# Kernel tuning notes

Measured on AMD Instinct MI355X. Metric: run time of the kernel, lower is better.

Reference implementation:

```python
import jax, jax.numpy as jnp
import numpy as np
import math

DIM = 1536
NH = 12
HD = 128          # head_dim
C = HD // 2       # 64 complex rope dims
MAX_ATTN = 15 * 880
EPS = 1e-6


def _rope_tables(max_len=1024, d=HD, theta=10000.0):
    # Wan rope_params: freqs = cat([rope(1024, d-4*(d//6)), rope(1024, 2*(d//6)), rope(1024, 2*(d//6))], dim=1)
    d0 = d - 4 * (d // 6)   # 44 -> 22 complex dims (F axis)
    d1 = 2 * (d // 6)       # 42 -> 21 complex dims (H and W axes)
    parts = []
    for dd in (d0, d1, d1):
        inv = 1.0 / theta ** (np.arange(0, dd, 2, dtype=np.float32) / dd)
        parts.append(np.outer(np.arange(max_len, dtype=np.float32), inv))
    ang = np.concatenate(parts, axis=1)                 # [1024, C]
    return np.stack([np.cos(ang), np.sin(ang)], -1)     # [1024, C, 2]


def rmsnorm(x, g, eps=EPS):
    return x * jax.lax.rsqrt(jnp.mean(x * x, axis=-1, keepdims=True) + eps) * g


def rope_apply(xq, f, h, w, freqs, start_frame):
    # xq: [B, S, N, D]; freqs: [1024, C, 2] cos/sin tables; S = f*h*w
    b, s, n, d = xq.shape
    c = d // 2
    s0 = c - 2 * (c // 3)   # F-axis complex dims (22)
    s1 = c // 3             # H/W-axis complex dims (21)
    cos, sin = freqs[..., 0], freqs[..., 1]

    def per_token(tab):
        tf = jnp.broadcast_to(tab[start_frame:start_frame + f, :s0][:, None, None, :], (f, h, w, s0))
        th = jnp.broadcast_to(tab[:h, s0:s0 + s1][None, :, None, :], (f, h, w, s1))
        tw = jnp.broadcast_to(tab[:w, s0 + s1:][None, None, :, :], (f, h, w, s1))
        return jnp.concatenate([tf, th, tw], -1).reshape(1, s, 1, c)

    pc, ps = per_token(cos), per_token(sin)
    xr = xq.reshape(b, s, n, c, 2)
    re, im = xr[..., 0], xr[..., 1]
    out = jnp.stack([re * pc - im * ps, re * ps + im * pc], -1)
    return out.reshape(b, s, n, d)


def _forward(x, wq, bq, wk, bk, wv, bv, wo, bo, gq, gk, freqs, k_cache, v_cache, f, h, w, current_start):
    b, s, _ = x.shape
    frame_seqlen = h * w
    start_frame = current_start // frame_seqlen

    q = rmsnorm(x @ wq.T + bq, gq).reshape(b, s, NH, HD)
    k = rmsnorm(x @ wk.T + bk, gk).reshape(b, s, NH, HD)
    v = (x @ wv.T + bv).reshape(b, s, NH, HD)

    rq = rope_apply(q, f, h, w, freqs, start_frame)
    rk = rope_apply(k, f, h, w, freqs, start_frame)

    current_end = current_start + s
    # cache not full: append new keys/values at [current_start:current_end]
    k_cache = jax.lax.dynamic_update_slice(k_cache, rk, (0, current_start, 0, 0))
    v_cache = jax.lax.dynamic_update_slice(v_cache, v, (0, current_start, 0, 0))

    win_start = max(0, current_end - MAX_ATTN)
    kk = k_cache[:, win_start:current_end]   # [B, Lk, N, D]
    vv = v_cache[:, win_start:current_end]

    scale = 1.0 / math.sqrt(HD)
    scores = jnp.einsum('bqnd,bknd->bnqk', rq, kk) * scale
    attn = jax.nn.softmax(scores, axis=-1)
    out = jnp.einsum('bnqk,bknd->bqnd', attn, vv).reshape(b, s, DIM)
    return out @ wo.T + bo


def setup_inputs() -> dict:
    key = jax.random.key(0)
    ks = jax.random.split(key, 8)
    B, S, CACHE = 1, 880, 18 * 880
    x = jax.random.normal(ks[0], (B, S, DIM), jnp.float32)

    def lin(k):
        k1, k2 = jax.random.split(k)
        wgt = jax.random.normal(k1, (DIM, DIM), jnp.float32) / math.sqrt(DIM)
        bia = jax.random.normal(k2, (DIM,), jnp.float32) * 0.01
        return wgt, bia

    wq, bq = lin(ks[1]); wk, bk = lin(ks[2]); wv, bv = lin(ks[3]); wo, bo = lin(ks[4])
    gq = jnp.ones((DIM,), jnp.float32)
    gk = jnp.ones((DIM,), jnp.float32)
    freqs = jnp.asarray(_rope_tables())
    k_cache = jax.random.normal(ks[5], (B, CACHE, NH, HD), jnp.float32) * 0.5
    v_cache = jax.random.normal(ks[6], (B, CACHE, NH, HD), jnp.float32) * 0.5
    grid_sizes = jnp.array([1, 22, 40], jnp.int32)  # (F, H, W), H*W = 880
    return dict(x=x, wq=wq, bq=bq, wk=wk, bk=bk, wv=wv, bv=bv, wo=wo, bo=bo,
                gq=gq, gk=gk, freqs=freqs, k_cache=k_cache, v_cache=v_cache,
                grid_sizes=grid_sizes, current_start=10560)


def reference(x, wq, bq, wk, bk, wv, bv, wo, bo, gq, gk, freqs, k_cache, v_cache, grid_sizes, current_start):
    f, h, w = (int(grid_sizes[0]), int(grid_sizes[1]), int(grid_sizes[2]))
    return _forward(x, wq, bq, wk, bk, wv, bv, wo, bo, gq, gk, freqs,
                    k_cache, v_cache, f, h, w, int(current_start))
```

## Files before the change

kernel.cpp:

```cpp
#include <hip/hip_runtime.h>

#define NHEADS 12
#define HDIM 128
#define MODEL_DIM 1536
#define MAX_ATTN_W 13200
#define NSPLIT 18

typedef unsigned short u16;
typedef unsigned int u32;
typedef float f32x4 __attribute__((ext_vector_type(4)));
typedef float f32x16 __attribute__((ext_vector_type(16)));
typedef __bf16 bf16x8 __attribute__((ext_vector_type(8)));

static __device__ __forceinline__ u16 f2bf(float f) {
  union { __bf16 h; u16 u; } cv;
  cv.h = (__bf16)f;
  return cv.u;
}
static __device__ __forceinline__ float bf2f(u16 u) {
  union { u32 u; float f; } cv;
  cv.u = ((u32)u) << 16;
  return cv.f;
}
static __device__ __forceinline__ u32 pk2(float a, float b) {
  return (u32)f2bf(a) | ((u32)f2bf(b) << 16);
}
static __device__ __forceinline__ void gload_lds16(const void* g, void* l) {
  __builtin_amdgcn_global_load_lds(
      (const __attribute__((address_space(1))) unsigned int*)g,
      (__attribute__((address_space(3))) unsigned int*)l, 16, 0, 0);
}

__launch_bounds__(256)
__global__ void k_prep(const float* __restrict__ x, int nx4,
                       const float* __restrict__ wq, const float* __restrict__ wk,
                       const float* __restrict__ wv, const float* __restrict__ wo, int nw4,
                       u16* __restrict__ xb, u16* __restrict__ wqb, u16* __restrict__ wkb,
                       u16* __restrict__ wvb, u16* __restrict__ wob,
                       const float* __restrict__ kc, const float* __restrict__ vc,
                       u16* __restrict__ K_all, u16* __restrict__ VT,
                       const int* __restrict__ csp, int S, int KVcap) {
  const int tid = threadIdx.x;
  const int which = blockIdx.y;

  if (which <= 4) {
    const float* src = (which == 0) ? x : (which == 1) ? wq : (which == 2) ? wk
                       : (which == 3) ? wv : wo;
    u16* dst = (which == 0) ? xb : (which == 1) ? wqb : (which == 2) ? wkb
               : (which == 3) ? wvb : wob;
    const int n4 = (which == 0) ? nx4 : nw4;
    for (int i = blockIdx.x * 256 + tid; i < n4; i += gridDim.x * 256) {
      float4 v = ((const float4*)src)[i];
      ((uint2*)dst)[i] = make_uint2(pk2(v.x, v.y), pk2(v.z, v.w));
    }
    return;
  }

  const int cs = csp[0];
  const int ce = cs + S;
  int wst = ce - MAX_ATTN_W; if (wst < 0) wst = 0;
  const int oldlen = cs - wst;

  if (which == 5) {
    const long per = (long)oldlen * 16;
    const long total = per * NHEADS;
    for (long c = blockIdx.x * 256L + tid; c < total; c += (long)gridDim.x * 256) {
      int n = (int)(c / per);
      long r = c - (long)n * per;
      int jo = (int)(r >> 4);
      int dc = ((int)r & 15) * 8;
      const float* s = kc + ((size_t)(wst + jo) * NHEADS + n) * HDIM + dc;
      float4 a = *(const float4*)s;
      float4 b = *(const float4*)(s + 4);
      uint4 o;
      o.x = pk2(a.x, a.y);
      o.y = pk2(a.z, a.w);
      o.z = pk2(b.x, b.y);
      o.w = pk2(b.z, b.w);
      *(uint4*)(K_all + ((size_t)n * KVcap + jo) * HDIM + dc) = o;
    }
    return;
  }

  __shared__ u16 tile[64][130];
  const int njb = (KVcap + 63) >> 6;
  const int bx = blockIdx.x;
  if (bx >= njb * NHEADS) return;
  const int n = bx / njb;
  const int j0 = (bx - n * njb) * 64;
  if (j0 >= oldlen) return;

  #pragma unroll
  for (int i = 0; i < 8; i++) {
    int idx = tid + 256 * i;
    int jr = idx >> 5;
    int dc = (idx & 31) * 4;
    float4 v = make_float4(0.f, 0.f, 0.f, 0.f);
    if (j0 + jr < oldlen)
      v = *(const float4*)(vc + ((size_t)(wst + j0 + jr) * NHEADS + n) * HDIM + dc);
    *(u32*)&tile[jr][dc] = pk2(v.x, v.y);
    *(u32*)&tile[jr][dc + 2] = pk2(v.z, v.w);
  }
  __syncthreads();

  const int d = tid >> 1;
  const int jh = (tid & 1) * 32;
  alignas(16) u16 buf[32];
  #pragma unroll
  for (int jr = 0; jr < 32; jr++) buf[jr] = tile[jh + jr][d];
  u16* dst = VT + ((size_t)n * HDIM + d) * KVcap + j0 + jh;
  if (j0 + jh + 32 <= oldlen) {
    #pragma unroll
    for (int c = 0; c < 4; c++)
      *(uint4*)(dst + c * 8) = *(const uint4*)&buf[c * 8];
  } else {
    for (int jr = 0; jr < 32 && j0 + jh + jr < oldlen; jr++) dst[jr] = buf[jr];
  }
}

__launch_bounds__(256)
__global__ void k_gemm_o128(const u16* __restrict__ A, const u16* __restrict__ B,
                            const float* __restrict__ bias, float* __restrict__ out,
                            int M, int N, int K) {
  __shared__ __align__(16) u16 Al[2][128][40];
  __shared__ __align__(16) u16 Bl[2][128][40];
  const int n0 = blockIdx.y * 128;
  const int tid = threadIdx.x;
  const int wid = tid >> 6, l = tid & 63, l31 = l & 31, hi = l >> 5;
  const int wr = wid >> 1, wc = wid & 1;
  const int m0 = blockIdx.x * 128;
  f32x16 acc[2][2];
  #pragma unroll
  for (int mt = 0; mt < 2; mt++)
    #pragma unroll
    for (int nt = 0; nt < 2; nt++)
      #pragma unroll
      for (int j = 0; j < 16; j++) acc[mt][nt][j] = 0.f;
  const int row = tid >> 2, colc = (tid & 3) * 8;
  const u16* Ar0 = A + (size_t)(m0 + row) * K + colc;
  const u16* Ar1 = A + (size_t)(m0 + row + 64) * K + colc;
  const u16* Br0 = B + (size_t)(n0 + row) * K + colc;
  const u16* Br1 = B + (size_t)(n0 + row + 64) * K + colc;

  uint4 ra0, ra1, ra2, ra3, rb0, rb1, rb2, rb3;
  auto loadA = [&](int k0) {
    ra0 = *(const uint4*)(Ar0 + k0); ra1 = *(const uint4*)(Ar1 + k0);
    ra2 = *(const uint4*)(Br0 + k0); ra3 = *(const uint4*)(Br1 + k0);
  };
  auto loadB = [&](int k0) {
    rb0 = *(const uint4*)(Ar0 + k0); rb1 = *(const uint4*)(Ar1 + k0);
    rb2 = *(const uint4*)(Br0 + k0); rb3 = *(const uint4*)(Br1 + k0);
  };
  auto mfma_step = [&](int p) {
    #pragma unroll
    for (int ks = 0; ks < 2; ks++) {
      bf16x8 af[2], bfr[2];
      #pragma unroll
      for (int mt = 0; mt < 2; mt++)
        af[mt] = *(const bf16x8*)&Al[p][wr * 64 + mt * 32 + l31][ks * 16 + hi * 8];
      #pragma unroll
      for (int nt = 0; nt < 2; nt++)
        bfr[nt] = *(const bf16x8*)&Bl[p][wc * 64 + nt * 32 + l31][ks * 16 + hi * 8];
      #pragma unroll
      for (int mt = 0; mt < 2; mt++)
        #pragma unroll
        for (int nt = 0; nt < 2; nt++)
          acc[mt][nt] = __builtin_amdgcn_mfma_f32_32x32x16_bf16(af[mt], bfr[nt], acc[mt][nt], 0, 0, 0);
    }
  };

  const int nk = K / 32;
  loadA(0);
  for (int t = 0; t < nk; t += 2) {
    const int k0 = t * 32;
    if (t + 1 < nk) loadB(k0 + 32);
    __builtin_amdgcn_sched_barrier(0);
    if (t + 1 < nk) asm volatile("s_waitcnt vmcnt(4)" ::: "memory");
    else            asm volatile("s_waitcnt vmcnt(0)" ::: "memory");
    __builtin_amdgcn_sched_barrier(0);
    *(uint4*)&Al[0][row][colc] = ra0;
    *(uint4*)&Al[0][row + 64][colc] = ra1;
    *(uint4*)&Bl[0][row][colc] = ra2;
    *(uint4*)&Bl[0][row + 64][colc] = ra3;
    asm volatile("s_waitcnt lgkmcnt(0)" ::: "memory");
    __builtin_amdgcn_s_barrier();
    __builtin_amdgcn_sched_barrier(0);
    mfma_step(0);
    if (t + 2 < nk) loadA(k0 + 64);
    __builtin_amdgcn_sched_barrier(0);
    if (t + 2 < nk) asm volatile("s_waitcnt vmcnt(4)" ::: "memory");
    else            asm volatile("s_waitcnt vmcnt(0)" ::: "memory");
    __builtin_amdgcn_sched_barrier(0);
    *(uint4*)&Al[1][row][colc] = rb0;
    *(uint4*)&Al[1][row + 64][colc] = rb1;
    *(uint4*)&Bl[1][row][colc] = rb2;
    *(uint4*)&Bl[1][row + 64][colc] = rb3;
    asm volatile("s_waitcnt lgkmcnt(0)" ::: "memory");
    __builtin_amdgcn_s_barrier();
    __builtin_amdgcn_sched_barrier(0);
    mfma_step(1);
  }
  #pragma unroll
  for (int mt = 0; mt < 2; mt++)
    #pragma unroll
    for (int nt = 0; nt < 2; nt++) {
      const int col = n0 + wc * 64 + nt * 32 + l31;
      const float bb = bias[col];
      #pragma unroll
      for (int r = 0; r < 16; r++) {
        int rowo = m0 + wr * 64 + mt * 32 + (r & 3) + 8 * (r >> 2) + 4 * hi;
        if (rowo < M) out[(size_t)rowo * N + col] = acc[mt][nt][r] + bb;
      }
    }
}

__launch_bounds__(256)
__global__ void k_gemm_qkv128(const u16* __restrict__ A,
                              const u16* __restrict__ B0, const u16* __restrict__ B1,
                              const u16* __restrict__ B2,
                              const float* __restrict__ bias0, const float* __restrict__ bias1,
                              const float* __restrict__ bias2,
                              float* __restrict__ o0, float* __restrict__ o1, float* __restrict__ o2,
                              int M, int N, int K) {
  __shared__ __align__(16) u16 Al[2][128][40];
  __shared__ __align__(16) u16 Bl[2][128][40];
  const int nblk = N / 128;
  const int which = blockIdx.y / nblk;
  const int n0 = (blockIdx.y % nblk) * 128;
  const u16* B = (which == 0) ? B0 : ((which == 1) ? B1 : B2);
  const float* bias = (which == 0) ? bias0 : ((which == 1) ? bias1 : bias2);
  float* out = (which == 0) ? o0 : ((which == 1) ? o1 : o2);
  const int tid = threadIdx.x;
  const int wid = tid >> 6, l = tid & 63, l31 = l & 31, hi = l >> 5;
  const int wr = wid >> 1, wc = wid & 1;
  const int m0 = blockIdx.x * 128;
  f32x16 acc[2][2];
  #pragma unroll
  for (int mt = 0; mt < 2; mt++)
    #pragma unroll
    for (int nt = 0; nt < 2; nt++)
      #pragma unroll
      for (int j = 0; j < 16; j++) acc[mt][nt][j] = 0.f;
  const int row = tid >> 2, colc = (tid & 3) * 8;
  const u16* Ar0 = A + (size_t)(m0 + row) * K + colc;
  const u16* Ar1 = A + (size_t)(m0 + row + 64) * K + colc;
  const u16* Br0 = B + (size_t)(n0 + row) * K + colc;
  const u16* Br1 = B + (size_t)(n0 + row + 64) * K + colc;

  uint4 ra0, ra1, ra2, ra3, rb0, rb1, rb2, rb3;
  auto loadA = [&](int k0) {
    ra0 = *(const uint4*)(Ar0 + k0); ra1 = *(const uint4*)(Ar1 + k0);
    ra2 = *(const uint4*)(Br0 + k0); ra3 = *(const uint4*)(Br1 + k0);
  };
  auto loadB = [&](int k0) {
    rb0 = *(const uint4*)(Ar0 + k0); rb1 = *(const uint4*)(Ar1 + k0);
    rb2 = *(const uint4*)(Br0 + k0); rb3 = *(const uint4*)(Br1 + k0);
  };
  auto mfma_step = [&](int p) {
    #pragma unroll
    for (int ks = 0; ks < 2; ks++) {
      bf16x8 af[2], bfr[2];
      #pragma unroll
      for (int mt = 0; mt < 2; mt++)
        af[mt] = *(const bf16x8*)&Al[p][wr * 64 + mt * 32 + l31][ks * 16 + hi * 8];
      #pragma unroll
      for (int nt = 0; nt < 2; nt++)
        bfr[nt] = *(const bf16x8*)&Bl[p][wc * 64 + nt * 32 + l31][ks * 16 + hi * 8];
      #pragma unroll
      for (int mt = 0; mt < 2; mt++)
        #pragma unroll
        for (int nt = 0; nt < 2; nt++)
          acc[mt][nt] = __builtin_amdgcn_mfma_f32_32x32x16_bf16(af[mt], bfr[nt], acc[mt][nt], 0, 0, 0);
    }
  };

  const int nk = K / 32;
  loadA(0);
  for (int t = 0; t < nk; t += 2) {
    const int k0 = t * 32;
    if (t + 1 < nk) loadB(k0 + 32);
    __builtin_amdgcn_sched_barrier(0);
    if (t + 1 < nk) asm volatile("s_waitcnt vmcnt(4)" ::: "memory");
    else            asm volatile("s_waitcnt vmcnt(0)" ::: "memory");
    __builtin_amdgcn_sched_barrier(0);
    *(uint4*)&Al[0][row][colc] = ra0;
    *(uint4*)&Al[0][row + 64][colc] = ra1;
    *(uint4*)&Bl[0][row][colc] = ra2;
    *(uint4*)&Bl[0][row + 64][colc] = ra3;
    asm volatile("s_waitcnt lgkmcnt(0)" ::: "memory");
    __builtin_amdgcn_s_barrier();
    __builtin_amdgcn_sched_barrier(0);
    mfma_step(0);
    if (t + 2 < nk) loadA(k0 + 64);
    __builtin_amdgcn_sched_barrier(0);
    if (t + 2 < nk) asm volatile("s_waitcnt vmcnt(4)" ::: "memory");
    else            asm volatile("s_waitcnt vmcnt(0)" ::: "memory");
    __builtin_amdgcn_sched_barrier(0);
    *(uint4*)&Al[1][row][colc] = rb0;
    *(uint4*)&Al[1][row + 64][colc] = rb1;
    *(uint4*)&Bl[1][row][colc] = rb2;
    *(uint4*)&Bl[1][row + 64][colc] = rb3;
    asm volatile("s_waitcnt lgkmcnt(0)" ::: "memory");
    __builtin_amdgcn_s_barrier();
    __builtin_amdgcn_sched_barrier(0);
    mfma_step(1);
  }
  #pragma unroll
  for (int mt = 0; mt < 2; mt++)
    #pragma unroll
    for (int nt = 0; nt < 2; nt++) {
      const int col = n0 + wc * 64 + nt * 32 + l31;
      const float bb = bias[col];
      #pragma unroll
      for (int r = 0; r < 16; r++) {
        int rowo = m0 + wr * 64 + mt * 32 + (r & 3) + 8 * (r >> 2) + 4 * hi;
        if (rowo < M) out[(size_t)rowo * N + col] = acc[mt][nt][r] + bb;
      }
    }
}

__launch_bounds__(256)
__global__ void k_norm_rope(const float* __restrict__ qp, const float* __restrict__ kp,
                            const float* __restrict__ vp, const float* __restrict__ gq,
                            const float* __restrict__ gk, const float* __restrict__ freqs,
                            const int* __restrict__ gs, const int* __restrict__ csp,
                            int S, int KVcap,
                            u16* __restrict__ rq, u16* __restrict__ K_all,
                            u16* __restrict__ VT) {
  const int t = blockIdx.x;
  const int tid = threadIdx.x;
  const float* q = qp + (size_t)t * MODEL_DIM;
  const float* k = kp + (size_t)t * MODEL_DIM;
  const float* v = vp + (size_t)t * MODEL_DIM;
  float sq = 0.f, sk = 0.f;
  for (int j = tid; j < MODEL_DIM; j += 256) {
    float a = q[j]; sq += a * a;
    float b = k[j]; sk += b * b;
  }
  #pragma unroll
  for (int off = 32; off > 0; off >>= 1) {
    sq += __shfl_down(sq, off, 64);
    sk += __shfl_down(sk, off, 64);
  }
  __shared__ float red[8];
  int wv_ = tid >> 6, l = tid & 63;
  if (l == 0) { red[wv_] = sq; red[4 + wv_] = sk; }
  __syncthreads();
  sq = red[0] + red[1] + red[2] + red[3];
  sk = red[4] + red[5] + red[6] + red[7];
  const float rq_s = rsqrtf(sq * (1.0f / MODEL_DIM) + 1e-6f) * 0.12751744f;
  const float rk_s = rsqrtf(sk * (1.0f / MODEL_DIM) + 1e-6f);

  const int cs = csp[0];
  const int h = gs[1], ww = gs[2];
  const int hw = h * ww;
  const int sf = cs / hw;
  const int fi = t / hw;
  const int rr = t - fi * hw;
  const int hi = rr / ww;
  const int wi = rr - hi * ww;
  const int ce = cs + S;
  int wst = ce - MAX_ATTN_W; if (wst < 0) wst = 0;
  const int jj = cs + t - wst;

  for (int p = tid; p < NHEADS * 64; p += 256) {
    int n = p >> 6, c = p & 63;
    int pos = (c < 22) ? (sf + fi) : ((c < 43) ? hi : wi);
    float cv = freqs[(pos * 64 + c) * 2];
    float sv = freqs[(pos * 64 + c) * 2 + 1];
    int j0 = n * HDIM + 2 * c;
    float qr = q[j0] * rq_s * gq[j0];
    float qi = q[j0 + 1] * rq_s * gq[j0 + 1];
    *(u32*)(rq + ((size_t)n * S + t) * HDIM + 2 * c) = pk2(qr * cv - qi * sv, qr * sv + qi * cv);
    float kr = k[j0] * rk_s * gk[j0];
    float ki = k[j0 + 1] * rk_s * gk[j0 + 1];
    *(u32*)(K_all + ((size_t)n * KVcap + jj) * HDIM + 2 * c) = pk2(kr * cv - ki * sv, kr * sv + ki * cv);
  }
  for (int j = tid; j < MODEL_DIM; j += 256) {
    int n = j >> 7, d = j & 127;
    VT[((size_t)n * HDIM + d) * KVcap + jj] = f2bf(v[j]);
  }
}

__launch_bounds__(256, 2)
__global__ void k_attn_split(const u16* __restrict__ rq, const u16* __restrict__ K_all,
                             const u16* __restrict__ VT,
                             u16* __restrict__ po, float* __restrict__ pm, float* __restrict__ pl,
                             const int* __restrict__ csp, int S, int KVcap, int nqb) {
  __shared__ __align__(16) u16 Klds[2][64][128];
  __shared__ __align__(16) u16 Vlds[2][128][64];

  const int tid = threadIdx.x;
  const int wid = tid >> 6;
  const int l = tid & 63;
  const int l31 = l & 31;
  const int hi = l >> 5;
  const int swz = (l31 & 7) << 3;

  const int bx = blockIdx.x;
  const int xcd = bx & 7;
  const int j = bx >> 3;
  const int cl = j / nqb;
  const int qb = j - cl * nqb;
  const int chunkid = cl * 8 + xcd;
  const int head = chunkid / NSPLIT;
  const int split = chunkid - head * NSPLIT;
  const int q0 = qb * 128;

  const int cs = csp[0];
  const int ce = cs + S;
  int wst = ce - MAX_ATTN_W; if (wst < 0) wst = 0;
  const int KV = ce - wst;
  const int chunk = (((KV + NSPLIT - 1) / NSPLIT) + 63) & ~63;
  const int kstart = split * chunk;
  int kend = kstart + chunk; if (kend > KV) kend = KV;

  const size_t pbase = ((size_t)head * NSPLIT + split) * S;
  const int qrow = q0 + wid * 32 + l31;

  if (kstart >= kend) {
    if (qrow < S && hi == 0) { pm[pbase + qrow] = -3.0e38f; pl[pbase + qrow] = 0.f; }
    return;
  }

  bf16x8 qf[8];
  if (qrow < S) {
    const u16* qp = rq + ((size_t)head * S + qrow) * HDIM;
    #pragma unroll
    for (int ds = 0; ds < 8; ds++) qf[ds] = *(const bf16x8*)(qp + ds * 16 + hi * 8);
  } else {
    #pragma unroll
    for (int ds = 0; ds < 8; ds++)
      #pragma unroll
      for (int i = 0; i < 8; i++) qf[ds][i] = (__bf16)0.0f;
  }

  f32x16 o[4];
  #pragma unroll
  for (int dt = 0; dt < 4; dt++)
    #pragma unroll
    for (int j2 = 0; j2 < 16; j2++) o[dt][j2] = 0.f;
  float m_ = -3.0e38f, lsum_ = 0.f;

  const u16* Kh = K_all + (size_t)head * KVcap * HDIM;
  const u16* Vh = VT + (size_t)head * HDIM * KVcap;

  int krow_i[4], kcol_i[4], vd_i[4], vcol_i[4];
  #pragma unroll
  for (int i = 0; i < 4; i++) {
    int kr_ = (wid * 4 + i) * 4 + (l >> 4);
    krow_i[i] = kr_;
    kcol_i[i] = (((l & 15) ^ (kr_ & 7)) << 3);
    int vd_ = (wid * 4 + i) * 8 + (l >> 3);
    vd_i[i] = vd_;
    vcol_i[i] = (((l & 7) ^ (vd_ & 7)) << 3);
  }

  const int ntiles = (kend - kstart + 63) >> 6;

  auto issue_tile = [&](int p, int key0) {
    u16* kbase = &Klds[p][0][0] + (wid * 4) * 512;
    u16* vbase = &Vlds[p][0][0] + (wid * 4) * 512;
    #pragma unroll
    for (int i = 0; i < 4; i++)
      gload_lds16(Kh + (size_t)(key0 + krow_i[i]) * HDIM + kcol_i[i], kbase + i * 512);
    #pragma unroll
    for (int i = 0; i < 4; i++)
      gload_lds16(Vh + (size_t)vd_i[i] * KVcap + key0 + vcol_i[i], vbase + i * 512);
  };

  issue_tile(0, kstart);

  for (int t = 0; t < ntiles; t++) {
    const int key0 = kstart + (t << 6);
    const int cur = t & 1;

    if (t + 1 < ntiles) {
      issue_tile(cur ^ 1, key0 + 64);
      __builtin_amdgcn_sched_barrier(0);
      asm volatile("s_waitcnt vmcnt(8)" ::: "memory");
    } else {
      asm volatile("s_waitcnt vmcnt(0)" ::: "memory");
    }
    __builtin_amdgcn_s_barrier();
    __builtin_amdgcn_sched_barrier(0);

    f32x16 s[2];
    __builtin_amdgcn_s_setprio(1);
    #pragma unroll
    for (int kt = 0; kt < 2; kt++) {
      #pragma unroll
      for (int j2 = 0; j2 < 16; j2++) s[kt][j2] = 0.f;
      #pragma unroll
      for (int ds = 0; ds < 8; ds++) {
        bf16x8 kf = *(const bf16x8*)&Klds[cur][kt * 32 + l31][(ds * 16 + hi * 8) ^ swz];
        s[kt] = __builtin_amdgcn_mfma_f32_32x32x16_bf16(kf, qf[ds], s[kt], 0, 0, 0);
      }
    }
    __builtin_amdgcn_s_setprio(0);

    float tm = -3.0e38f;
    if (key0 + 64 <= kend) {
      #pragma unroll
      for (int kt = 0; kt < 2; kt++)
        #pragma unroll
        for (int r = 0; r < 16; r++) tm = fmaxf(tm, s[kt][r]);
    } else {
      #pragma unroll
      for (int kt = 0; kt < 2; kt++) {
        const int rem = kend - key0 - kt * 32;
        #pragma unroll
        for (int r = 0; r < 16; r++) {
          const int off = (r & 3) + 8 * (r >> 2) + 4 * hi;
          float v = (off < rem) ? s[kt][r] : -3.0e38f;
          s[kt][r] = v;
          tm = fmaxf(tm, v);
        }
      }
    }
    tm = fmaxf(tm, __shfl_xor(tm, 32, 64));

    if (!__all(tm <= m_ + 8.0f)) {
      float nm = fmaxf(m_, tm);
      float alpha = exp2f(m_ - nm);
      m_ = nm;
      lsum_ *= alpha;
      #pragma unroll
      for (int dt = 0; dt < 4; dt++)
        #pragma unroll
        for (int j2 = 0; j2 < 16; j2++) o[dt][j2] *= alpha;
    }

    float rs = 0.f;
    u32 w[2][8];
    #pragma unroll
    for (int kt = 0; kt < 2; kt++)
      #pragma unroll
      for (int j2 = 0; j2 < 8; j2++) {
        float p0 = exp2f(s[kt][2 * j2] - m_);
        float p1 = exp2f(s[kt][2 * j2 + 1] - m_);
        rs += p0 + p1;
        w[kt][j2] = pk2(p0, p1);
      }
    rs += __shfl_xor(rs, 32, 64);
    lsum_ += rs;

    union { u32 u[4]; bf16x8 v; } pf[2][2];
    #pragma unroll
    for (int kt = 0; kt < 2; kt++) {
      u32 xw[8];
      #pragma unroll
      for (int j2 = 0; j2 < 8; j2++) xw[j2] = __shfl_xor(w[kt][j2], 32, 64);
      pf[kt][0].u[0] = hi ? xw[2]    : w[kt][0];
      pf[kt][0].u[1] = hi ? xw[3]    : w[kt][1];
      pf[kt][0].u[2] = hi ? w[kt][2] : xw[0];
      pf[kt][0].u[3] = hi ? w[kt][3] : xw[1];
      pf[kt][1].u[0] = hi ? xw[6]    : w[kt][4];
      pf[kt][1].u[1] = hi ? xw[7]    : w[kt][5];
      pf[kt][1].u[2] = hi ? w[kt][6] : xw[4];
      pf[kt][1].u[3] = hi ? w[kt][7] : xw[5];
    }

    __builtin_amdgcn_s_setprio(1);
    #pragma unroll
    for (int dt = 0; dt < 4; dt++) {
      #pragma unroll
      for (int kt = 0; kt < 2; kt++)
        #pragma unroll
        for (int mm = 0; mm < 2; mm++) {
          bf16x8 vf = *(const bf16x8*)&Vlds[cur][dt * 32 + l31][(kt * 32 + mm * 16 + hi * 8) ^ swz];
          o[dt] = __builtin_amdgcn_mfma_f32_32x32x16_bf16(vf, pf[kt][mm].v, o[dt], 0, 0, 0);
        }
    }
    __builtin_amdgcn_s_setprio(0);

    __builtin_amdgcn_sched_barrier(0);
    __builtin_amdgcn_s_barrier();
  }

  if (qrow < S) {
    float rl = (lsum_ > 0.f) ? (1.0f / lsum_) : 0.f;
    u16* dst = po + (pbase + qrow) * HDIM;
    #pragma unroll
    for (int dt = 0; dt < 4; dt++)
      #pragma unroll
      for (int jj = 0; jj < 4; jj++) {
        u32 w0 = pk2(o[dt][4 * jj] * rl, o[dt][4 * jj + 1] * rl);
        u32 w1 = pk2(o[dt][4 * jj + 2] * rl, o[dt][4 * jj + 3] * rl);
        *(uint2*)(dst + dt * 32 + 8 * jj + 4 * hi) = make_uint2(w0, w1);
      }
    if (hi == 0) { pm[pbase + qrow] = m_; pl[pbase + qrow] = lsum_; }
  }
}

__launch_bounds__(256)
__global__ void k_attn_reduce(const u16* __restrict__ po, const float* __restrict__ pm,
                              const float* __restrict__ pl, u16* __restrict__ attn_out,
                              int S) {
  const int tb = blockIdx.x * 2 + (threadIdx.x >> 7);
  const int h = blockIdx.y;
  const int d = threadIdx.x & 127;
  if (tb >= S) return;
  float ms[NSPLIT];
  float M = -3.0e38f;
  #pragma unroll
  for (int s = 0; s < NSPLIT; s++) {
    ms[s] = pm[((size_t)h * NSPLIT + s) * S + tb];
    M = fmaxf(M, ms[s]);
  }
  float L = 0.f, acc = 0.f;
  #pragma unroll
  for (int s = 0; s < NSPLIT; s++) {
    float wgt = exp2f(ms[s] - M) * pl[((size_t)h * NSPLIT + s) * S + tb];
    L += wgt;
    acc += wgt * bf2f(po[(((size_t)h * NSPLIT + s) * S + tb) * HDIM + d]);
  }
  attn_out[(size_t)tb * MODEL_DIM + h * HDIM + d] = f2bf(acc / L);
}

extern "C" void kernel_launch(void* const* d_in, const int* in_sizes, int n_in,
                              void* d_out, int out_size, void* d_ws, size_t ws_size,
                              hipStream_t stream) {
  (void)n_in; (void)out_size; (void)ws_size;
  const float* x  = (const float*)d_in[0];
  const float* wq = (const float*)d_in[1];
  const float* bq = (const float*)d_in[2];
  const float* wk = (const float*)d_in[3];
  const float* bk = (const float*)d_in[4];
  const float* wv = (const float*)d_in[5];
  const float* bv = (const float*)d_in[6];
  const float* wo = (const float*)d_in[7];
  const float* bo = (const float*)d_in[8];
  const float* gq = (const float*)d_in[9];
  const float* gk = (const float*)d_in[10];
  const float* freqs = (const float*)d_in[11];
  const float* k_cache = (const float*)d_in[12];
  const float* v_cache = (const float*)d_in[13];
  const int* gs  = (const int*)d_in[14];
  const int* csp = (const int*)d_in[15];

  const int S = in_sizes[0] / MODEL_DIM;
  const int CACHE = in_sizes[12] / (NHEADS * HDIM);
  const int KVcap = (CACHE < MAX_ATTN_W) ? CACHE : MAX_ATTN_W;
  const int Mpad = (S + 127) & ~127;
  const int NQB = Mpad / 128;

  char* ws = (char*)d_ws;
  size_t off = 0;
  auto alloc = [&](size_t bytes) {
    char* p = ws + off;
    off += (bytes + 255) & ~(size_t)255;
    return p;
  };
  u16* xb   = (u16*)alloc((size_t)Mpad * MODEL_DIM * 2);
  u16* wqb  = (u16*)alloc((size_t)MODEL_DIM * MODEL_DIM * 2);
  u16* wkb  = (u16*)alloc((size_t)MODEL_DIM * MODEL_DIM * 2);
  u16* wvb  = (u16*)alloc((size_t)MODEL_DIM * MODEL_DIM * 2);
  u16* wob  = (u16*)alloc((size_t)MODEL_DIM * MODEL_DIM * 2);
  float* q_pre = (float*)alloc((size_t)S * MODEL_DIM * 4);
  float* k_pre = (float*)alloc((size_t)S * MODEL_DIM * 4);
  float* v_pre = (float*)alloc((size_t)S * MODEL_DIM * 4);
  u16* rqb   = (u16*)alloc((size_t)NHEADS * S * HDIM * 2);
  u16* K_all = (u16*)alloc((size_t)NHEADS * KVcap * HDIM * 2);
  u16* VT    = (u16*)alloc((size_t)NHEADS * HDIM * KVcap * 2);
  u16* attn_o = (u16*)alloc((size_t)Mpad * MODEL_DIM * 2);
  u16* po    = (u16*)alloc((size_t)NHEADS * NSPLIT * S * HDIM * 2);
  float* pm  = (float*)alloc((size_t)NHEADS * NSPLIT * S * 4);
  float* pl  = (float*)alloc((size_t)NHEADS * NSPLIT * S * 4);

  const int nx4 = S * MODEL_DIM / 4;
  const int nw4 = MODEL_DIM * MODEL_DIM / 4;
  const int njb = (KVcap + 63) / 64;
  int gx = njb * NHEADS;
  if (gx < (nw4 + 255) / 256) gx = (nw4 + 255) / 256;
  if (gx < (nx4 + 255) / 256) gx = (nx4 + 255) / 256;

  hipLaunchKernelGGL(k_prep, dim3(gx, 7), dim3(256), 0, stream,
                     x, nx4, wq, wk, wv, wo, nw4, xb, wqb, wkb, wvb, wob,
                     k_cache, v_cache, K_all, VT, csp, S, KVcap);

  hipLaunchKernelGGL(k_gemm_qkv128, dim3(Mpad / 128, 3 * MODEL_DIM / 128), dim3(256), 0, stream,
                     xb, wqb, wkb, wvb, bq, bk, bv, q_pre, k_pre, v_pre, S, MODEL_DIM, MODEL_DIM);

  hipLaunchKernelGGL(k_norm_rope, dim3(S), dim3(256), 0, stream,
                     q_pre, k_pre, v_pre, gq, gk, freqs, gs, csp, S, KVcap, rqb, K_all, VT);

  hipLaunchKernelGGL(k_attn_split, dim3(NQB * NHEADS * NSPLIT), dim3(256), 0, stream,
                     rqb, K_all, VT, po, pm, pl, csp, S, KVcap, NQB);

  hipLaunchKernelGGL(k_attn_reduce, dim3((S + 1) / 2, NHEADS), dim3(256), 0, stream,
                     po, pm, pl, attn_o, S);

  hipLaunchKernelGGL(k_gemm_o128, dim3(Mpad / 128, MODEL_DIM / 128), dim3(256), 0, stream,
                     attn_o, wob, bo, (float*)d_out, S, MODEL_DIM, MODEL_DIM);
}
```

Before: 280.3 us.

## Halve attention KV tile to 32 keys and raise occupancy to three blocks

Shrinks the split-KV attention inner tile from 64 to 32 keys, halving the K/V LDS double buffers and the per-tile score and probability registers. Launch bounds go from 2 to 3 blocks per CU, so more waves can hide memory latency. The V-transpose LDS layout gets a new swizzle for the 32-wide rows. In exchange there are twice as many loop iterations, each paying its own barrier, max/rescale check and shuffle overhead, and each tile gives less MFMA work to overlap with loads.

```diff
diff --git a/kernel.cpp b/kernel.cpp
--- a/kernel.cpp
+++ b/kernel.cpp
@@ -382,13 +382,13 @@
   }
 }
 
-__launch_bounds__(256, 2)
+__launch_bounds__(256, 3)
 __global__ void k_attn_split(const u16* __restrict__ rq, const u16* __restrict__ K_all,
                              const u16* __restrict__ VT,
                              u16* __restrict__ po, float* __restrict__ pm, float* __restrict__ pl,
                              const int* __restrict__ csp, int S, int KVcap, int nqb) {
-  __shared__ __align__(16) u16 Klds[2][64][128];
-  __shared__ __align__(16) u16 Vlds[2][128][64];
+  __shared__ __align__(16) u16 Klds[2][32][128];
+  __shared__ __align__(16) u16 Vlds[2][128][32];
 
   const int tid = threadIdx.x;
   const int wid = tid >> 6;
@@ -411,7 +411,7 @@
   const int ce = cs + S;
   int wst = ce - MAX_ATTN_W; if (wst < 0) wst = 0;
   const int KV = ce - wst;
-  const int chunk = (((KV + NSPLIT - 1) / NSPLIT) + 63) & ~63;
+  const int chunk = (((KV + NSPLIT - 1) / NSPLIT) + 31) & ~31;
   const int kstart = split * chunk;
   int kend = kstart + chunk; if (kend > KV) kend = KV;
 
@@ -445,77 +445,70 @@
   const u16* Kh = K_all + (size_t)head * KVcap * HDIM;
   const u16* Vh = VT + (size_t)head * HDIM * KVcap;
 
-  int krow_i[4], kcol_i[4], vd_i[4], vcol_i[4];
-  #pragma unroll
-  for (int i = 0; i < 4; i++) {
-    int kr_ = (wid * 4 + i) * 4 + (l >> 4);
+  int krow_i[2], kcol_i[2], vd_i[2], vcol_i[2];
+  #pragma unroll
+  for (int i = 0; i < 2; i++) {
+    int gi = wid * 2 + i;
+    int kr_ = gi * 4 + (l >> 4);
     krow_i[i] = kr_;
     kcol_i[i] = (((l & 15) ^ (kr_ & 7)) << 3);
-    int vd_ = (wid * 4 + i) * 8 + (l >> 3);
+    int vd_ = gi * 16 + (l >> 2);
     vd_i[i] = vd_;
-    vcol_i[i] = (((l & 7) ^ (vd_ & 7)) << 3);
-  }
-
-  const int ntiles = (kend - kstart + 63) >> 6;
+    vcol_i[i] = (((l & 3) ^ ((vd_ >> 1) & 3)) << 3);
+  }
+
+  const int ntiles = (kend - kstart + 31) >> 5;
 
   auto issue_tile = [&](int p, int key0) {
-    u16* kbase = &Klds[p][0][0] + (wid * 4) * 512;
-    u16* vbase = &Vlds[p][0][0] + (wid * 4) * 512;
-    #pragma unroll
-    for (int i = 0; i < 4; i++)
+    u16* kbase = &Klds[p][0][0] + (wid * 2) * 512;
+    u16* vbase = &Vlds[p][0][0] + (wid * 2) * 512;
+    #pragma unroll
+    for (int i = 0; i < 2; i++)
       gload_lds16(Kh + (size_t)(key0 + krow_i[i]) * HDIM + kcol_i[i], kbase + i * 512);
     #pragma unroll
-    for (int i = 0; i < 4; i++)
+    for (int i = 0; i < 2; i++)
       gload_lds16(Vh + (size_t)vd_i[i] * KVcap + key0 + vcol_i[i], vbase + i * 512);
   };
 
   issue_tile(0, kstart);
 
   for (int t = 0; t < ntiles; t++) {
-    const int key0 = kstart + (t << 6);
+    const int key0 = kstart + (t << 5);
     const int cur = t & 1;
 
     if (t + 1 < ntiles) {
-      issue_tile(cur ^ 1, key0 + 64);
+      issue_tile(cur ^ 1, key0 + 32);
       __builtin_amdgcn_sched_barrier(0);
-      asm volatile("s_waitcnt vmcnt(8)" ::: "memory");
+      asm volatile("s_waitcnt vmcnt(4)" ::: "memory");
     } else {
       asm volatile("s_waitcnt vmcnt(0)" ::: "memory");
     }
     __builtin_amdgcn_s_barrier();
     __builtin_amdgcn_sched_barrier(0);
 
-    f32x16 s[2];
+    f32x16 s;
     __builtin_amdgcn_s_setprio(1);
     #pragma unroll
-    for (int kt = 0; kt < 2; kt++) {
-      #pragma unroll
-      for (int j2 = 0; j2 < 16; j2++) s[kt][j2] = 0.f;
-      #pragma unroll
-      for (int ds = 0; ds < 8; ds++) {
-        bf16x8 kf = *(const bf16x8*)&Klds[cur][kt * 32 + l31][(ds * 16 + hi * 8) ^ swz];
-        s[kt] = __builtin_amdgcn_mfma_f32_32x32x16_bf16(kf, qf[ds], s[kt], 0, 0, 0);
-      }
+    for (int j2 = 0; j2 < 16; j2++) s[j2] = 0.f;
+    #pragma unroll
+    for (int ds = 0; ds < 8; ds++) {
+      bf16x8 kf = *(const bf16x8*)&Klds[cur][l31][(ds * 16 + hi * 8) ^ swz];
+      s = __builtin_amdgcn_mfma_f32_32x32x16_bf16(kf, qf[ds], s, 0, 0, 0);
     }
     __builtin_amdgcn_s_setprio(0);
 
     float tm = -3.0e38f;
-    if (key0 + 64 <= kend) {
-      #pragma unroll
-      for (int kt = 0; kt < 2; kt++)
-        #pragma unroll
-        for (int r = 0; r < 16; r++) tm = fmaxf(tm, s[kt][r]);
+    if (key0 + 32 <= kend) {
+      #pragma unroll
+      for (int r = 0; r < 16; r++) tm = fmaxf(tm, s[r]);
     } else {
-      #pragma unroll
-      for (int kt = 0; kt < 2; kt++) {
-        const int rem = kend - key0 - kt * 32;
-        #pragma unroll
-        for (int r = 0; r < 16; r++) {
-          const int off = (r & 3) + 8 * (r >> 2) + 4 * hi;
-          float v = (off < rem) ? s[kt][r] : -3.0e38f;
-          s[kt][r] = v;
-          tm = fmaxf(tm, v);
-        }
+      const int rem = kend - key0;
+      #pragma unroll
+      for (int r = 0; r < 16; r++) {
+        const int off = (r & 3) + 8 * (r >> 2) + 4 * hi;
+        float v = (off < rem) ? s[r] : -3.0e38f;
+        s[r] = v;
+        tm = fmaxf(tm, v);
       }
     }
     tm = fmaxf(tm, __shfl_xor(tm, 32, 64));
@@ -532,45 +525,42 @@
     }
 
     float rs = 0.f;
-    u32 w[2][8];
-    #pragma unroll
-    for (int kt = 0; kt < 2; kt++)
-      #pragma unroll
-      for (int j2 = 0; j2 < 8; j2++) {
-        float p0 = exp2f(s[kt][2 * j2] - m_);
-        float p1 = exp2f(s[kt][2 * j2 + 1] - m_);
-        rs += p0 + p1;
-        w[kt][j2] = pk2(p0, p1);
-      }
+    u32 w[8];
+    #pragma unroll
+    for (int j2 = 0; j2 < 8; j2++) {
+      float p0 = exp2f(s[2 * j2] - m_);
+      float p1 = exp2f(s[2 * j2 + 1] - m_);
+      rs += p0 + p1;
+      w[j2] = pk2(p0, p1);
+    }
     rs += __shfl_xor(rs, 32, 64);
     lsum_ += rs;
 
-    union { u32 u[4]; bf16x8 v; } pf[2][2];
-    #pragma unroll
-    for (int kt = 0; kt < 2; kt++) {
+    union { u32 u[4]; bf16x8 v; } pf[2];
+    {
       u32 xw[8];
       #pragma unroll
-      for (int j2 = 0; j2 < 8; j2++) xw[j2] = __shfl_xor(w[kt][j2], 32, 64);
-      pf[kt][0].u[0] = hi ? xw[2]    : w[kt][0];
-      pf[kt][0].u[1] = hi ? xw[3]    : w[kt][1];
-      pf[kt][0].u[2] = hi ? w[kt][2] : xw[0];
-      pf[kt][0].u[3] = hi ? w[kt][3] : xw[1];
-      pf[kt][1].u[0] = hi ? xw[6]    : w[kt][4];
-      pf[kt][1].u[1] = hi ? xw[7]    : w[kt][5];
-      pf[kt][1].u[2] = hi ? w[kt][6] : xw[4];
-      pf[kt][1].u[3] = hi ? w[kt][7] : xw[5];
+      for (int j2 = 0; j2 < 8; j2++) xw[j2] = __shfl_xor(w[j2], 32, 64);
+      pf[0].u[0] = hi ? xw[2] : w[0];
+      pf[0].u[1] = hi ? xw[3] : w[1];
+      pf[0].u[2] = hi ? w[2]  : xw[0];
+      pf[0].u[3] = hi ? w[3]  : xw[1];
+      pf[1].u[0] = hi ? xw[6] : w[4];
+      pf[1].u[1] = hi ? xw[7] : w[5];
+      pf[1].u[2] = hi ? w[6]  : xw[4];
+      pf[1].u[3] = hi ? w[7]  : xw[5];
     }
 
     __builtin_amdgcn_s_setprio(1);
     #pragma unroll
     for (int dt = 0; dt < 4; dt++) {
-      #pragma unroll
-      for (int kt = 0; kt < 2; kt++)
-        #pragma unroll
-        for (int mm = 0; mm < 2; mm++) {
-          bf16x8 vf = *(const bf16x8*)&Vlds[cur][dt * 32 + l31][(kt * 32 + mm * 16 + hi * 8) ^ swz];
-          o[dt] = __builtin_amdgcn_mfma_f32_32x32x16_bf16(vf, pf[kt][mm].v, o[dt], 0, 0, 0);
-        }
+      const int vrow = dt * 32 + l31;
+      const int vswz = ((vrow >> 1) & 3) << 3;
+      #pragma unroll
+      for (int mm = 0; mm < 2; mm++) {
+        bf16x8 vf = *(const bf16x8*)&Vlds[cur][vrow][(mm * 16 + hi * 8) ^ vswz];
+        o[dt] = __builtin_amdgcn_mfma_f32_32x32x16_bf16(vf, pf[mm].v, o[dt], 0, 0, 0);
+      }
     }
     __builtin_amdgcn_s_setprio(0);
 
```

After: 276.8 us (median of 2 runs). Within noise of the previous version (-1.2%).
